# Kernel optimization log

Measured on AMD Instinct MI355X. Metric: run time of the kernel, lower is better.

The kernel has to match this reference:

```python
import jax, jax.numpy as jnp
import numpy as np

NLAB = 21
B, T, D = 64, 512, 1024


def _crf_log_partition(logits, mask, transitions, start_t, end_t):
    # logits [B,T,n], mask [B,T] bool -> logZ [B]
    lT = jnp.swapaxes(logits, 0, 1)          # [T,B,n]
    mT = jnp.swapaxes(mask, 0, 1)            # [T,B]
    alpha0 = start_t[None, :] + lT[0]        # [B,n]

    def step(alpha, xm):
        emit, m = xm
        # inner[b, prev, next] = alpha[b,prev] + transitions[prev,next] + emit[b,next]
        inner = alpha[:, :, None] + transitions[None, :, :] + emit[:, None, :]
        new = jax.nn.logsumexp(inner, axis=1)
        return jnp.where(m[:, None], new, alpha), None

    alpha, _ = jax.lax.scan(step, alpha0, (lT[1:], mT[1:]))
    return jax.nn.logsumexp(alpha + end_t[None, :], axis=-1)


def _crf_joint_score(logits, tags, mask, transitions, start_t, end_t):
    # AllenNLP _joint_likelihood, vectorized. -> [B]
    maskf = mask.astype(logits.dtype)
    score = start_t[tags[:, 0]]
    trans_sc = transitions[tags[:, :-1], tags[:, 1:]]                      # [B,T-1]
    emit_sc = jnp.take_along_axis(logits, tags[:, :, None], axis=2)[..., 0]  # [B,T]
    score = score + jnp.sum(trans_sc * maskf[:, 1:], axis=1)
    score = score + jnp.sum(emit_sc[:, :-1] * maskf[:, :-1], axis=1)
    last_idx = jnp.sum(mask.astype(jnp.int32), axis=1) - 1                 # [B]
    last_tags = jnp.take_along_axis(tags, last_idx[:, None], axis=1)[:, 0]
    last_emit = jnp.take_along_axis(logits[:, -1, :], last_tags[:, None], axis=1)[:, 0]
    score = score + end_t[last_tags] + last_emit * maskf[:, -1]
    return score


def _viterbi(logits, mask, transitions, start_t, end_t):
    # -> best tags [B,T]
    lT = jnp.swapaxes(logits, 0, 1)
    mT = jnp.swapaxes(mask, 0, 1)
    alpha0 = start_t[None, :] + lT[0]

    def step(alpha, xm):
        emit, m = xm
        scores = alpha[:, :, None] + transitions[None, :, :]  # [B,prev,next]
        best = jnp.max(scores, axis=1) + emit
        bp = jnp.argmax(scores, axis=1)                       # [B,next]
        return jnp.where(m[:, None], best, alpha), bp

    alpha, bps = jax.lax.scan(step, alpha0, (lT[1:], mT[1:]))  # bps [T-1,B,n]
    last_tag = jnp.argmax(alpha + end_t[None, :], axis=-1)     # [B]

    def back(tag, bpm):
        bp, m = bpm
        prev = jnp.take_along_axis(bp, tag[:, None], axis=1)[:, 0]
        new_tag = jnp.where(m, prev, tag)
        return new_tag, new_tag

    _, rev = jax.lax.scan(back, last_tag, (bps[::-1], mT[1:][::-1]))
    tags = jnp.concatenate([rev[::-1], last_tag[None, :]], axis=0)  # [T,B]
    return jnp.swapaxes(tags, 0, 1)


def setup_inputs() -> dict:
    key = jax.random.key(0)
    ks = jax.random.split(key, 6)
    mlm_out = jax.random.normal(ks[0], (B, T, D), dtype=jnp.float32)
    mask = jnp.ones((B, T), dtype=bool)
    gold = jax.random.randint(ks[1], (B, T), 0, NLAB)
    W = jax.random.normal(ks[2], (NLAB, D), dtype=jnp.float32) * (1.0 / np.sqrt(D))
    b = jnp.zeros((NLAB,), dtype=jnp.float32)
    transitions = jax.random.normal(ks[3], (NLAB, NLAB), dtype=jnp.float32) * 0.1
    start_transitions = jax.random.normal(ks[4], (NLAB,), dtype=jnp.float32) * 0.1
    end_transitions = jax.random.normal(ks[5], (NLAB,), dtype=jnp.float32) * 0.1
    return {"mlm_out": mlm_out, "mask": mask, "gold": gold, "W": W, "b": b,
            "transitions": transitions, "start_transitions": start_transitions,
            "end_transitions": end_transitions}


def reference(mlm_out, mask, gold, W, b, transitions, start_transitions, end_transitions):
    logits = jnp.einsum('btd,nd->btn', mlm_out, W) + b  # hidden_to_label
    logZ = _crf_log_partition(logits, mask, transitions, start_transitions, end_transitions)
    joint = _crf_joint_score(logits, gold, mask, transitions, start_transitions, end_transitions)
    log_likelihood = jnp.sum(joint - logZ)
    loss = -log_likelihood * 1.0  # loss_weight = 1.0
    pred_tags = _viterbi(logits, mask, transitions, start_transitions, end_transitions)
    return logits, loss, pred_tags
```

## Files before the change

### kernel.cpp

```cpp
#include <hip/hip_runtime.h>
#include <stdint.h>

#define NLAB 21
#define BB 64
#define TT 512
#define DD 1024
#define OFF_LOSS (BB*TT*NLAB)
#define OFF_TAGS (OFF_LOSS + 1)

#define LOG2E 1.4426950408889634f
#define LN2   0.6931471805599453f

#define NC 8
#define MATSZ (NLAB*NLAB)
#define WS_ML 0
#define WS_MV (BB*NC*MATSZ)
#define WS_BS (2*BB*NC*MATSZ)

static __device__ __forceinline__ float readlane_f(float v, int i) {
    return __int_as_float(__builtin_amdgcn_readlane(__float_as_int(v), i));
}

#define GK 64
#define XS_PITCH 65
__global__ __launch_bounds__(256) void gemm_logits(
    const float* __restrict__ X, const float* __restrict__ W,
    const float* __restrict__ bias, float* __restrict__ out)
{
    const int tid = threadIdx.x;
    const int tok = tid & 63;
    const int kq  = tid >> 6;
    const int tb  = blockIdx.x * 64;

    __shared__ float smem[GK * XS_PITCH];

    float acc[NLAB];
#pragma unroll
    for (int n = 0; n < NLAB; ++n) acc[n] = 0.f;

    for (int ch = 0; ch < DD / GK; ++ch) {
        const int kc = ch * GK;
        __syncthreads();
#pragma unroll
        for (int u = 0; u < 4; ++u) {
            int r  = (tid >> 4) + u * 16;
            int c4 = tid & 15;
            float4 v = *(const float4*)(X + (size_t)(tb + r) * DD + kc + c4 * 4);
            smem[(c4*4 + 0) * XS_PITCH + r] = v.x;
            smem[(c4*4 + 1) * XS_PITCH + r] = v.y;
            smem[(c4*4 + 2) * XS_PITCH + r] = v.z;
            smem[(c4*4 + 3) * XS_PITCH + r] = v.w;
        }
        __syncthreads();

        float xv[16];
#pragma unroll
        for (int kk = 0; kk < 16; ++kk)
            xv[kk] = smem[(kq * 16 + kk) * XS_PITCH + tok];

        int kidx = kc + kq * 16;
        int vkidx;
        asm("v_mov_b32 %0, %1" : "=v"(vkidx) : "s"(kidx));
        const float* Wk = W + vkidx;
#pragma unroll
        for (int n = 0; n < NLAB; ++n) {
            float a = acc[n];
#pragma unroll
            for (int g = 0; g < 4; ++g) {
                float4 wv = *(const float4*)(Wk + (size_t)n * DD + g * 4);
                a = fmaf(xv[g*4 + 0], wv.x, a);
                a = fmaf(xv[g*4 + 1], wv.y, a);
                a = fmaf(xv[g*4 + 2], wv.z, a);
                a = fmaf(xv[g*4 + 3], wv.w, a);
            }
            acc[n] = a;
        }
    }

    __syncthreads();
    if (kq > 0) {
        float* r = smem + ((kq - 1) * 64 + tok) * NLAB;
#pragma unroll
        for (int n = 0; n < NLAB; ++n) r[n] = acc[n];
    }
    __syncthreads();
    if (kq == 0) {
        const float* r0 = smem + tok * NLAB;
        const float* r1 = smem + (64 + tok) * NLAB;
        const float* r2 = smem + (128 + tok) * NLAB;
        float* o = out + (size_t)(tb + tok) * NLAB;
#pragma unroll
        for (int n = 0; n < NLAB; ++n)
            o[n] = acc[n] + r0[n] + r1[n] + r2[n] + bias[n];
    }
    if (blockIdx.x == 0 && tid == 0) out[OFF_LOSS] = 0.f;
}

__global__ __launch_bounds__(64) void crf_chunks(
    const float* __restrict__ logits, const float* __restrict__ trans,
    const float* __restrict__ startT, float* __restrict__ ws)
{
    const int lane = threadIdx.x;
    const int role = blockIdx.x & 1;
    const int y    = blockIdx.x >> 1;
    const int b    = y / 50;
    const int r    = y - b * 50;

    int grp = lane / 21; if (grp > 2) grp = 2;
    int j   = lane - grp * 21; if (j > 20) j = 20;
    const bool act = lane < 63;

    int c, i;
    if (r == 0) { c = 0; i = 0; }
    else { c = 1 + (r - 1) / 7; int wg = (r - 1) % 7; i = wg * 3 + grp; }
    const int t0 = c * 64;

    const float* lt = logits + ((size_t)b * TT + t0) * NLAB + j;

    __shared__ __align__(16) float vb[3][24];
    __shared__ __align__(16) float eb[3][24];

    float v;
    if (r == 0) v = startT[j] + lt[0];
    else        v = trans[i * NLAB + j] + lt[0];

    float em[4];
#pragma unroll
    for (int u = 0; u < 4; ++u) em[u] = lt[(1 + u) * NLAB];

    if (role == 0) {
        float Ecol[NLAB];
#pragma unroll
        for (int k = 0; k < NLAB; ++k) Ecol[k] = expf(trans[k * NLAB + j]);

        for (int s0 = 1; s0 <= 63; s0 += 4) {
#pragma unroll
            for (int u = 0; u < 4; ++u) {
                int s = s0 + u;
                if (s <= 63) {
                    float emit = em[u];
                    if (s + 4 <= 63) em[u] = lt[(s + 4) * NLAB];
                    float m = readlane_f(v, 0);
                    float e = exp2f((v - m) * LOG2E);
                    if (act) eb[grp][j] = e;
                    const float4* ep = (const float4*)eb[grp];
                    float4 E0 = ep[0], E1 = ep[1], E2 = ep[2], E3 = ep[3], E4 = ep[4];
                    float e20 = eb[grp][20];
                    float sA = E0.x*Ecol[0];
                    sA = fmaf(E0.y,Ecol[1],sA); sA = fmaf(E0.z,Ecol[2],sA);
                    sA = fmaf(E0.w,Ecol[3],sA); sA = fmaf(E1.x,Ecol[4],sA);
                    sA = fmaf(E1.y,Ecol[5],sA); sA = fmaf(E1.z,Ecol[6],sA);
                    float sB = E1.w*Ecol[7];
                    sB = fmaf(E2.x,Ecol[8],sB);  sB = fmaf(E2.y,Ecol[9],sB);
                    sB = fmaf(E2.z,Ecol[10],sB); sB = fmaf(E2.w,Ecol[11],sB);
                    sB = fmaf(E3.x,Ecol[12],sB); sB = fmaf(E3.y,Ecol[13],sB);
                    float sC = E3.z*Ecol[14];
                    sC = fmaf(E3.w,Ecol[15],sC); sC = fmaf(E4.x,Ecol[16],sC);
                    sC = fmaf(E4.y,Ecol[17],sC); sC = fmaf(E4.z,Ecol[18],sC);
                    sC = fmaf(E4.w,Ecol[19],sC); sC = fmaf(e20, Ecol[20],sC);
                    float ss = (sA + sB) + sC;
                    float na = m + log2f(ss) * LN2 + emit;
                    v = act ? na : v;
                }
            }
        }
        if (act && (r > 0 || grp == 0))
            ws[WS_ML + ((size_t)(b * NC + c) * NLAB + i) * NLAB + j] = v;
    } else {
        float Tcol[NLAB];
#pragma unroll
        for (int k = 0; k < NLAB; ++k) Tcol[k] = trans[k * NLAB + j];

        for (int s0 = 1; s0 <= 63; s0 += 4) {
#pragma unroll
            for (int u = 0; u < 4; ++u) {
                int s = s0 + u;
                if (s <= 63) {
                    float emit = em[u];
                    if (s + 4 <= 63) em[u] = lt[(s + 4) * NLAB];
                    if (act) vb[grp][j] = v;
                    const float4* rp = (const float4*)vb[grp];
                    float4 R0 = rp[0], R1 = rp[1], R2 = rp[2], R3 = rp[3], R4 = rp[4];
                    float r20 = vb[grp][20];
                    float m0 = fmaxf(fmaxf(R0.x+Tcol[0],  R0.y+Tcol[1]),
                                     fmaxf(R0.z+Tcol[2],  R0.w+Tcol[3]));
                    float m1 = fmaxf(fmaxf(R1.x+Tcol[4],  R1.y+Tcol[5]),
                                     fmaxf(R1.z+Tcol[6],  R1.w+Tcol[7]));
                    float m2 = fmaxf(fmaxf(R2.x+Tcol[8],  R2.y+Tcol[9]),
                                     fmaxf(R2.z+Tcol[10], R2.w+Tcol[11]));
                    float m3 = fmaxf(fmaxf(R3.x+Tcol[12], R3.y+Tcol[13]),
                                     fmaxf(R3.z+Tcol[14], R3.w+Tcol[15]));
                    float m4 = fmaxf(fmaxf(R4.x+Tcol[16], R4.y+Tcol[17]),
                                     fmaxf(R4.z+Tcol[18], R4.w+Tcol[19]));
                    float best = fmaxf(fmaxf(fmaxf(m0, m1), fmaxf(m2, m3)),
                                       fmaxf(m4, r20 + Tcol[20]));
                    v = best + emit;
                }
            }
        }
        if (act && (r > 0 || grp == 0))
            ws[WS_MV + ((size_t)(b * NC + c) * NLAB + i) * NLAB + j] = v;
    }
}

__global__ __launch_bounds__(64) void crf_combine(
    const float* __restrict__ logits, const int* __restrict__ gold,
    const float* __restrict__ trans, const float* __restrict__ startT,
    const float* __restrict__ endT, float* __restrict__ ws,
    float* __restrict__ out)
{
    const int lane = threadIdx.x;
    const int role = blockIdx.x & 1;
    const int b    = blockIdx.x >> 1;
    const int jc   = (lane < NLAB) ? lane : (NLAB - 1);
    const bool act = lane < NLAB;

    if (role == 0) {
        const float* lg = logits + (size_t)b * TT * NLAB;
        float js = 0.f;
        for (int t = lane; t < TT; t += 64) {
            int g = gold[b*TT + t];
            js += lg[t*NLAB + g];
            if (t < TT-1) js += trans[g*NLAB + gold[b*TT + t + 1]];
        }
#pragma unroll
        for (int off = 32; off >= 1; off >>= 1)
            js += __shfl_xor(js, off, 64);
        js += startT[gold[b*TT]] + endT[gold[b*TT + TT - 1]];

        float a = act ? ws[WS_ML + (size_t)(b * NC) * MATSZ + jc] : -3.0e38f;
#pragma unroll
        for (int c = 1; c < NC; ++c) {
            const float* Mc = ws + WS_ML + (size_t)(b * NC + c) * MATSZ;
            float col[NLAB];
#pragma unroll
            for (int k = 0; k < NLAB; ++k) col[k] = Mc[k * NLAB + jc];
            float m  = readlane_f(a, 0);
            float e  = exp2f((a - m) * LOG2E);
            float m2 = col[0];
            float s0 = 0.f, s1 = 0.f, s2 = 0.f;
#pragma unroll
            for (int k = 0; k < 7; ++k) {
                s0 = fmaf(readlane_f(e, k),      exp2f((col[k]      - m2) * LOG2E), s0);
                s1 = fmaf(readlane_f(e, k + 7),  exp2f((col[k + 7]  - m2) * LOG2E), s1);
                s2 = fmaf(readlane_f(e, k + 14), exp2f((col[k + 14] - m2) * LOG2E), s2);
            }
            float s = (s0 + s1) + s2;
            float na = m + m2 + log2f(s) * LN2;
            a = act ? na : a;
        }
        float v = act ? (a + endT[jc]) : -3.0e38f;
        float mm = v;
#pragma unroll
        for (int off = 32; off >= 1; off >>= 1)
            mm = fmaxf(mm, __shfl_xor(mm, off, 64));
        float se = act ? exp2f((v - mm) * LOG2E) : 0.f;
#pragma unroll
        for (int off = 32; off >= 1; off >>= 1)
            se += __shfl_xor(se, off, 64);
        float logZ = mm + log2f(se) * LN2;
        if (lane == 0) atomicAdd(out + OFF_LOSS, logZ - js);
    } else {
        float A = act ? ws[WS_MV + (size_t)(b * NC) * MATSZ + jc] : -3.0e38f;
        int ent[NC];
#pragma unroll
        for (int c = 1; c < NC; ++c) {
            const float* Vc = ws + WS_MV + (size_t)(b * NC + c) * MATSZ;
            float col[NLAB];
#pragma unroll
            for (int k = 0; k < NLAB; ++k) col[k] = Vc[k * NLAB + jc];
            float best = readlane_f(A, 0) + col[0];
            int bi = 0;
#pragma unroll
            for (int k = 1; k < NLAB; ++k) {
                float cand = readlane_f(A, k) + col[k];
                if (cand > best) { best = cand; bi = k; }
            }
            ent[c] = bi;
            A = act ? best : A;
        }
        float v = act ? (A + endT[jc]) : -3.0e38f;
        int idx = jc;
#pragma unroll
        for (int off = 32; off >= 1; off >>= 1) {
            float ov = __shfl_xor(v, off, 64);
            int   oi = __shfl_xor(idx, off, 64);
            if (ov > v || (ov == v && oi < idx)) { v = ov; idx = oi; }
        }
        int s[NC];
        s[NC-1] = idx;
#pragma unroll
        for (int c = NC - 1; c >= 1; --c)
            s[c-1] = __builtin_amdgcn_readlane(ent[c], s[c]);
        int* BS = (int*)(ws + WS_BS);
        if (lane == 0) {
#pragma unroll
            for (int c = 0; c < NC; ++c) BS[b * NC + c] = s[c];
        }
    }
}

__global__ __launch_bounds__(64) void crf_tags(
    const float* __restrict__ logits, const float* __restrict__ trans,
    const float* __restrict__ startT, const float* __restrict__ ws,
    float* __restrict__ out)
{
    const int lane = threadIdx.x;
    const int b    = blockIdx.x >> 3;
    const int c    = blockIdx.x & 7;
    const int jc   = (lane < NLAB) ? lane : (NLAB - 1);
    const bool act = lane < NLAB;
    const int t0   = c * 64;

    const int* BS = (const int*)(ws + WS_BS);
    const int exitS = BS[b * NC + c];

    const float* lt = logits + ((size_t)b * TT + t0) * NLAB + jc;

    __shared__ __align__(16) float vb[24];
    __shared__ uint8_t bp[64][24];

    float Tcol[NLAB];
#pragma unroll
    for (int k = 0; k < NLAB; ++k) Tcol[k] = trans[k * NLAB + jc];

    float v;
    if (c == 0) v = startT[jc] + lt[0];
    else { int entry = BS[b * NC + c - 1]; v = trans[entry * NLAB + jc] + lt[0]; }

    float em[4];
#pragma unroll
    for (int u = 0; u < 4; ++u) em[u] = lt[(1 + u) * NLAB];

    for (int s0 = 1; s0 <= 63; s0 += 4) {
#pragma unroll
        for (int u = 0; u < 4; ++u) {
            int s = s0 + u;
            if (s <= 63) {
                float emit = em[u];
                if (s + 4 <= 63) em[u] = lt[(s + 4) * NLAB];
                if (act) vb[jc] = v;
                const float4* rp = (const float4*)vb;
                float4 R0 = rp[0], R1 = rp[1], R2 = rp[2], R3 = rp[3], R4 = rp[4];
                float r20 = vb[20];
                float cv[NLAB];
                cv[0]=R0.x+Tcol[0];  cv[1]=R0.y+Tcol[1];  cv[2]=R0.z+Tcol[2];
                cv[3]=R0.w+Tcol[3];  cv[4]=R1.x+Tcol[4];  cv[5]=R1.y+Tcol[5];
                cv[6]=R1.z+Tcol[6];  cv[7]=R1.w+Tcol[7];  cv[8]=R2.x+Tcol[8];
                cv[9]=R2.y+Tcol[9];  cv[10]=R2.z+Tcol[10]; cv[11]=R2.w+Tcol[11];
                cv[12]=R3.x+Tcol[12]; cv[13]=R3.y+Tcol[13]; cv[14]=R3.z+Tcol[14];
                cv[15]=R3.w+Tcol[15]; cv[16]=R4.x+Tcol[16]; cv[17]=R4.y+Tcol[17];
                cv[18]=R4.z+Tcol[18]; cv[19]=R4.w+Tcol[19]; cv[20]=r20+Tcol[20];
                float v11[11]; int i11[11];
#pragma unroll
                for (int q = 0; q < 10; ++q) {
                    bool tk = cv[2*q+1] > cv[2*q];
                    v11[q] = tk ? cv[2*q+1] : cv[2*q];
                    i11[q] = tk ? (2*q+1) : (2*q);
                }
                v11[10] = cv[20]; i11[10] = 20;
                float v6[6]; int i6[6];
#pragma unroll
                for (int q = 0; q < 5; ++q) {
                    bool tk = v11[2*q+1] > v11[2*q];
                    v6[q] = tk ? v11[2*q+1] : v11[2*q];
                    i6[q] = tk ? i11[2*q+1] : i11[2*q];
                }
                v6[5] = v11[10]; i6[5] = i11[10];
                float v3[3]; int i3[3];
#pragma unroll
                for (int q = 0; q < 3; ++q) {
                    bool tk = v6[2*q+1] > v6[2*q];
                    v3[q] = tk ? v6[2*q+1] : v6[2*q];
                    i3[q] = tk ? i6[2*q+1] : i6[2*q];
                }
                bool tka = v3[1] > v3[0];
                float vbm = tka ? v3[1] : v3[0];
                int   ibm = tka ? i3[1] : i3[0];
                bool tkb = v3[2] > vbm;
                float best = tkb ? v3[2] : vbm;
                int   bi   = tkb ? i3[2] : ibm;

                if (act) bp[s][jc] = (uint8_t)bi;
                v = best + emit;
            }
        }
    }

    int rowv[64];
#pragma unroll
    for (int u = 0; u < 64; ++u)
        rowv[u] = bp[u][(lane < 24) ? lane : 0];
    int cur = exitS;
    int tagreg = 0;
    if (lane == 63) tagreg = cur;
#pragma unroll
    for (int u = 63; u >= 1; --u) {
        cur = __builtin_amdgcn_readlane(rowv[u], cur);
        if (lane == u - 1) tagreg = cur;
    }
    out[OFF_TAGS + (size_t)b * TT + t0 + lane] = (float)tagreg;
}

extern "C" void kernel_launch(void* const* d_in, const int* in_sizes, int n_in,
                              void* d_out, int out_size, void* d_ws, size_t ws_size,
                              hipStream_t stream)
{
    const float* X     = (const float*)d_in[0];
    const int*   gold  = (const int*)d_in[2];
    const float* W     = (const float*)d_in[3];
    const float* bias  = (const float*)d_in[4];
    const float* trans = (const float*)d_in[5];
    const float* st    = (const float*)d_in[6];
    const float* en    = (const float*)d_in[7];
    float* out = (float*)d_out;
    float* ws  = (float*)d_ws;

    hipLaunchKernelGGL(gemm_logits, dim3(512),  dim3(256), 0, stream, X, W, bias, out);
    hipLaunchKernelGGL(crf_chunks,  dim3(6400), dim3(64),  0, stream, out, trans, st, ws);
    hipLaunchKernelGGL(crf_combine, dim3(128),  dim3(64),  0, stream, out, gold, trans, st, en, ws, out);
    hipLaunchKernelGGL(crf_tags,    dim3(512),  dim3(64),  0, stream, out, trans, st, ws, out);
}
```

Baseline: 396.2 us.

## Compute logits GEMM with split-bf16 MFMA instead of FP32 FMA

Replaces the LDS-staged FP32 FMA logits GEMM with a matrix-core version built on 16x16x32 bf16 MFMA. A new prep kernel splits W into high and low bf16 halves in the workspace. The GEMM splits X on the fly and accumulates three MFMA products (hi*hi, hi*lo, lo*hi) to keep near-FP32 accuracy. The goal is to cut the arithmetic and LDS cost of the GEMM so it becomes bound by reading X. In exchange it adds an extra launch, pads N from 21 to 32, and introduces small rounding differences from the dropped lo*lo term.

Result: faster. 331.6 us (-16.3%).

```diff
diff --git a/kernel.cpp b/kernel.cpp
--- a/kernel.cpp
+++ b/kernel.cpp
@@ -21,77 +21,88 @@
     return __int_as_float(__builtin_amdgcn_readlane(__float_as_int(v), i));
 }
 
-#define GK 64
-#define XS_PITCH 65
+using bf16x8 = __attribute__((ext_vector_type(8))) short;
+using f32x4  = __attribute__((ext_vector_type(4))) float;
+
+static __device__ __forceinline__ unsigned short f2bf(float f) {
+    unsigned int u = __float_as_uint(f);
+    u = u + 0x7fffu + ((u >> 16) & 1u);
+    return (unsigned short)(u >> 16);
+}
+static __device__ __forceinline__ float bf2f(unsigned short h) {
+    return __uint_as_float(((unsigned int)h) << 16);
+}
+
+__global__ __launch_bounds__(256) void gemm_prep_w(
+    const float* __restrict__ W, float* __restrict__ ws)
+{
+    int idx = blockIdx.x * 256 + threadIdx.x;
+    int n = idx >> 10, k = idx & 1023;
+    float v = (n < NLAB) ? W[n * DD + k] : 0.f;
+    unsigned short h = f2bf(v);
+    unsigned short l = f2bf(v - bf2f(h));
+    unsigned short* wh = (unsigned short*)ws;
+    wh[idx] = h;
+    wh[32 * 1024 + idx] = l;
+}
+
 __global__ __launch_bounds__(256) void gemm_logits(
-    const float* __restrict__ X, const float* __restrict__ W,
+    const float* __restrict__ X, const float* __restrict__ ws,
     const float* __restrict__ bias, float* __restrict__ out)
 {
-    const int tid = threadIdx.x;
-    const int tok = tid & 63;
-    const int kq  = tid >> 6;
-    const int tb  = blockIdx.x * 64;
-
-    __shared__ float smem[GK * XS_PITCH];
-
-    float acc[NLAB];
-#pragma unroll
-    for (int n = 0; n < NLAB; ++n) acc[n] = 0.f;
-
-    for (int ch = 0; ch < DD / GK; ++ch) {
-        const int kc = ch * GK;
-        __syncthreads();
-#pragma unroll
-        for (int u = 0; u < 4; ++u) {
-            int r  = (tid >> 4) + u * 16;
-            int c4 = tid & 15;
-            float4 v = *(const float4*)(X + (size_t)(tb + r) * DD + kc + c4 * 4);
-            smem[(c4*4 + 0) * XS_PITCH + r] = v.x;
-            smem[(c4*4 + 1) * XS_PITCH + r] = v.y;
-            smem[(c4*4 + 2) * XS_PITCH + r] = v.z;
-            smem[(c4*4 + 3) * XS_PITCH + r] = v.w;
-        }
-        __syncthreads();
-
-        float xv[16];
-#pragma unroll
-        for (int kk = 0; kk < 16; ++kk)
-            xv[kk] = smem[(kq * 16 + kk) * XS_PITCH + tok];
-
-        int kidx = kc + kq * 16;
-        int vkidx;
-        asm("v_mov_b32 %0, %1" : "=v"(vkidx) : "s"(kidx));
-        const float* Wk = W + vkidx;
-#pragma unroll
-        for (int n = 0; n < NLAB; ++n) {
-            float a = acc[n];
-#pragma unroll
-            for (int g = 0; g < 4; ++g) {
-                float4 wv = *(const float4*)(Wk + (size_t)n * DD + g * 4);
-                a = fmaf(xv[g*4 + 0], wv.x, a);
-                a = fmaf(xv[g*4 + 1], wv.y, a);
-                a = fmaf(xv[g*4 + 2], wv.z, a);
-                a = fmaf(xv[g*4 + 3], wv.w, a);
-            }
-            acc[n] = a;
-        }
-    }
-
-    __syncthreads();
-    if (kq > 0) {
-        float* r = smem + ((kq - 1) * 64 + tok) * NLAB;
-#pragma unroll
-        for (int n = 0; n < NLAB; ++n) r[n] = acc[n];
-    }
-    __syncthreads();
-    if (kq == 0) {
-        const float* r0 = smem + tok * NLAB;
-        const float* r1 = smem + (64 + tok) * NLAB;
-        const float* r2 = smem + (128 + tok) * NLAB;
-        float* o = out + (size_t)(tb + tok) * NLAB;
-#pragma unroll
-        for (int n = 0; n < NLAB; ++n)
-            o[n] = acc[n] + r0[n] + r1[n] + r2[n] + bias[n];
+    const int tid  = threadIdx.x;
+    const int lane = tid & 63;
+    const int wv   = tid >> 6;
+    const int tb   = blockIdx.x * 64 + wv * 16;
+    const int mr   = lane & 15;
+    const int kc   = lane >> 4;
+
+    const float*  xp  = X + (size_t)(tb + mr) * DD + kc * 8;
+    const unsigned short* wh = (const unsigned short*)ws;
+    const unsigned short* wl = wh + 32 * 1024;
+    const unsigned short* bh0 = wh + mr * 1024 + kc * 8;
+    const unsigned short* bl0 = wl + mr * 1024 + kc * 8;
+    const unsigned short* bh1 = bh0 + 16 * 1024;
+    const unsigned short* bl1 = bl0 + 16 * 1024;
+
+    f32x4 aM0 = {0.f,0.f,0.f,0.f}, aC0 = {0.f,0.f,0.f,0.f};
+    f32x4 aM1 = {0.f,0.f,0.f,0.f}, aC1 = {0.f,0.f,0.f,0.f};
+
+#pragma unroll 4
+    for (int ks = 0; ks < 32; ++ks) {
+        float4 xa = *(const float4*)(xp + ks * 32);
+        float4 xb = *(const float4*)(xp + ks * 32 + 4);
+        float xs[8] = {xa.x, xa.y, xa.z, xa.w, xb.x, xb.y, xb.z, xb.w};
+        bf16x8 xh, xl;
+#pragma unroll
+        for (int j = 0; j < 8; ++j) {
+            unsigned short h = f2bf(xs[j]);
+            xh[j] = (short)h;
+            xl[j] = (short)f2bf(xs[j] - bf2f(h));
+        }
+        bf16x8 w0h = *(const bf16x8*)(bh0 + ks * 32);
+        bf16x8 w0l = *(const bf16x8*)(bl0 + ks * 32);
+        bf16x8 w1h = *(const bf16x8*)(bh1 + ks * 32);
+        bf16x8 w1l = *(const bf16x8*)(bl1 + ks * 32);
+
+        aM0 = __builtin_amdgcn_mfma_f32_16x16x32_bf16(xh, w0h, aM0, 0, 0, 0);
+        aC0 = __builtin_amdgcn_mfma_f32_16x16x32_bf16(xh, w0l, aC0, 0, 0, 0);
+        aC0 = __builtin_amdgcn_mfma_f32_16x16x32_bf16(xl, w0h, aC0, 0, 0, 0);
+        aM1 = __builtin_amdgcn_mfma_f32_16x16x32_bf16(xh, w1h, aM1, 0, 0, 0);
+        aC1 = __builtin_amdgcn_mfma_f32_16x16x32_bf16(xh, w1l, aC1, 0, 0, 0);
+        aC1 = __builtin_amdgcn_mfma_f32_16x16x32_bf16(xl, w1h, aC1, 0, 0, 0);
+    }
+
+    const int n0 = mr;
+    const int n1 = mr + 16;
+    const float b0 = bias[n0];
+    const float b1 = (n1 < NLAB) ? bias[n1] : 0.f;
+#pragma unroll
+    for (int r = 0; r < 4; ++r) {
+        int trow = tb + kc * 4 + r;
+        float* o = out + (size_t)trow * NLAB;
+        o[n0] = aM0[r] + aC0[r] + b0;
+        if (n1 < NLAB) o[n1] = aM1[r] + aC1[r] + b1;
     }
     if (blockIdx.x == 0 && tid == 0) out[OFF_LOSS] = 0.f;
 }
@@ -416,7 +427,8 @@
     float* out = (float*)d_out;
     float* ws  = (float*)d_ws;
 
-    hipLaunchKernelGGL(gemm_logits, dim3(512),  dim3(256), 0, stream, X, W, bias, out);
+    hipLaunchKernelGGL(gemm_prep_w, dim3(128),  dim3(256), 0, stream, W, ws);
+    hipLaunchKernelGGL(gemm_logits, dim3(512),  dim3(256), 0, stream, X, ws, bias, out);
     hipLaunchKernelGGL(crf_chunks,  dim3(6400), dim3(64),  0, stream, out, trans, st, ws);
     hipLaunchKernelGGL(crf_combine, dim3(128),  dim3(64),  0, stream, out, gold, trans, st, en, ws, out);
     hipLaunchKernelGGL(crf_tags,    dim3(512),  dim3(64),  0, stream, out, trans, st, ws, out);
```
